# Optimization experiments

Hardware: AMD Instinct MI355X
Metric: run time of the kernel (lower is better)

Reference implementation:

```python
import jax, jax.numpy as jnp
import numpy as np

N_NODES = 50000


def gcn_conv(x, W, b, src, dst, norm, n):
    # x: [N, Fin]; W: [Fin, Fout]; src/dst/norm: [E+N] (self-loops included)
    h = x @ W                                   # dense transform first (PyG order)
    msg = h[src] * norm[:, None]                # gather + per-edge scale
    out = jax.ops.segment_sum(msg, dst, num_segments=n)  # scatter-add aggregate
    return out + b


def setup_inputs() -> dict:
    key = jax.random.key(0)
    k1, k2, k3, k4 = jax.random.split(key, 4)
    F_IN, H, C, E = 64, 64, 16, 800000
    x = jax.random.normal(k1, (N_NODES, F_IN), dtype=jnp.float32)
    edge_index = jax.random.randint(k2, (2, E), 0, N_NODES, dtype=jnp.int64)
    W1 = jax.random.normal(k3, (F_IN, H), dtype=jnp.float32) * (1.0 / np.sqrt(F_IN))
    b1 = jnp.zeros((H,), dtype=jnp.float32)
    W2 = jax.random.normal(k4, (H, C), dtype=jnp.float32) * (1.0 / np.sqrt(H))
    b2 = jnp.zeros((C,), dtype=jnp.float32)
    return {"x": x, "edge_index": edge_index, "W1": W1, "b1": b1, "W2": W2, "b2": b2}


def reference(x, edge_index, W1, b1, W2, b2):
    n = x.shape[0]
    loops = jnp.arange(n, dtype=edge_index.dtype)
    src = jnp.concatenate([edge_index[0], loops])  # GCN adds self-loops
    dst = jnp.concatenate([edge_index[1], loops])
    # symmetric normalization: deg^{-1/2}[src] * deg^{-1/2}[dst], deg over dst
    deg = jax.ops.segment_sum(jnp.ones_like(dst, dtype=x.dtype), dst, num_segments=n)
    dinv = jax.lax.rsqrt(deg)  # deg >= 1 due to self-loops
    norm = dinv[src] * dinv[dst]
    h = gcn_conv(x, W1, b1, src, dst, norm, n)
    h = jax.nn.relu(h)
    out = gcn_conv(h, W2, b2, src, dst, norm, n)
    return out
```

## Files before the change

kernel.cpp:

```cpp
#include <hip/hip_runtime.h>

#define N_NODES 50000
#define N_EDGES 800000
#define F1 64
#define F2 16
#define NBINS 196
#define BIN_SHIFT 8
#define EPB 8192
#define NSB ((N_EDGES + EPB - 1) / EPB)
#define TBW 200
#define STAGE_MAX 6144
#define G1_ROWS 32
#define G1_NB ((N_NODES + G1_ROWS - 1) / G1_ROWS)

typedef _Float16 half_t;
typedef __attribute__((ext_vector_type(8))) _Float16 half8;
typedef __attribute__((ext_vector_type(4))) _Float16 half4;

__global__ void __launch_bounds__(256) k_bs_gemm1(
        const int* __restrict__ src, const int* __restrict__ dst,
        unsigned* __restrict__ pairs, int* __restrict__ table,
        const float* __restrict__ x, const float* __restrict__ W1,
        half_t* __restrict__ h0h) {
    __shared__ int smem[1024 + EPB];
    int t = threadIdx.x;

    if (blockIdx.x < NSB) {
        int* hist    = smem;
        int* loff    = smem + 256;
        int* lcur    = smem + 512;
        int* scanbuf = smem + 768;
        unsigned* stage = (unsigned*)(smem + 1024);
        int blk = blockIdx.x;
        int e0 = blk * EPB;
        int eend = min(e0 + EPB, N_EDGES);
        int n = eend - e0;

        for (int i = t; i < NBINS; i += 256) hist[i] = 0;
        __syncthreads();
        for (int e = e0 + t; e < eend; e += 256)
            atomicAdd(&hist[dst[e] >> BIN_SHIFT], 1);
        __syncthreads();
        int v = (t < NBINS) ? hist[t] : 0;
        scanbuf[t] = v;
        __syncthreads();
        for (int s = 1; s < 256; s <<= 1) {
            int u = (t >= s) ? scanbuf[t - s] : 0;
            __syncthreads();
            scanbuf[t] += u;
            __syncthreads();
        }
        if (t < NBINS) { loff[t] = scanbuf[t] - v; lcur[t] = scanbuf[t] - v; }
        if (t == 0) loff[NBINS] = n;
        __syncthreads();
        for (int e = e0 + t; e < eend; e += 256) {
            int d = dst[e];
            int b = d >> BIN_SHIFT;
            int pos = atomicAdd(&lcur[b], 1);
            stage[pos] = (unsigned)src[e] | ((unsigned)(d & 255) << 16);
        }
        if (t <= NBINS) table[blk * TBW + t] = loff[t];
        __syncthreads();
        for (int i = t; i < n; i += 256) pairs[e0 + i] = stage[i];
    } else {
        float* Ws = (float*)smem;
        int bid = blockIdx.x - NSB;
        int lane = t & 63, wid = t >> 6;
        for (int i = t; i < F1 * F1; i += 256) Ws[i] = W1[i];
        int row0 = bid * G1_ROWS + wid * 8;
        float xv[8], acc[8];
#pragma unroll
        for (int r = 0; r < 8; ++r) {
            int row = row0 + r;
            xv[r] = (row < N_NODES) ? x[row * F1 + lane] : 0.f;
            acc[r] = 0.f;
        }
        __syncthreads();
#pragma unroll
        for (int k = 0; k < F1; ++k) {
            float w = Ws[k * F1 + lane];
#pragma unroll
            for (int r = 0; r < 8; ++r) {
                float xs = __int_as_float(
                    __builtin_amdgcn_readlane(__float_as_int(xv[r]), k));
                acc[r] = fmaf(xs, w, acc[r]);
            }
        }
#pragma unroll
        for (int r = 0; r < 8; ++r) {
            int row = row0 + r;
            if (row < N_NODES) h0h[row * F1 + lane] = (half_t)acc[r];
        }
    }
}

__global__ void __launch_bounds__(256) k_binsort(
        const int* __restrict__ table, const unsigned* __restrict__ pairs,
        float* __restrict__ dinv, int* __restrict__ node_start,
        unsigned short* __restrict__ csr) {
    __shared__ int segoff[NSB];
    __shared__ int segcnt[NSB];
    __shared__ int segdst[NSB];
    __shared__ int scanbuf[256];
    __shared__ int hist[256];
    __shared__ int lcur[256];
    __shared__ unsigned stage[STAGE_MAX];
    __shared__ unsigned short sorted[STAGE_MAX];
    int t = threadIdx.x, b = blockIdx.x;
    int lane = t & 63, wid = t >> 6;

    int c = 0, colsum = 0;
    if (t < NSB) {
        int o = table[t * TBW + b];
        segoff[t] = o;
        colsum = o;
        c = table[t * TBW + b + 1] - o;
        segcnt[t] = c;
    }
    scanbuf[t] = c;
    hist[t] = colsum;
    __syncthreads();
    for (int s = 1; s < 256; s <<= 1) {
        int u  = (t >= s) ? scanbuf[t - s] : 0;
        int u2 = (t >= s) ? hist[t - s] : 0;
        __syncthreads();
        scanbuf[t] += u;
        hist[t] += u2;
        __syncthreads();
    }
    if (t < NSB) segdst[t] = scanbuf[t] - c;
    int n = scanbuf[255];
    int bstart = hist[255];
    __syncthreads();
    hist[t] = 0;
    __syncthreads();

    for (int k = wid; k < NSB; k += 4) {
        int sc = segcnt[k], base = k * EPB + segoff[k], sd = segdst[k];
        for (int i = lane; i < sc; i += 64) stage[sd + i] = pairs[base + i];
    }
    __syncthreads();

    for (int i = t; i < n; i += 256) atomicAdd(&hist[stage[i] >> 16], 1);
    __syncthreads();

    int lo = b << BIN_SHIFT;
    int nb = min(256, N_NODES - lo);
    int hv = hist[t];
    if (t < nb) dinv[lo + t] = rsqrtf(1.0f + (float)hv);
    scanbuf[t] = hv;
    __syncthreads();
    for (int s = 1; s < 256; s <<= 1) {
        int u = (t >= s) ? scanbuf[t - s] : 0;
        __syncthreads();
        scanbuf[t] += u;
        __syncthreads();
    }
    int pr = scanbuf[t] - hv;
    if (t < nb) node_start[lo + t] = bstart + pr;
    if (b == NBINS - 1 && t == 0) node_start[N_NODES] = N_EDGES;
    lcur[t] = pr;
    __syncthreads();

    for (int i = t; i < n; i += 256) {
        unsigned p = stage[i];
        int pos = atomicAdd(&lcur[p >> 16], 1);
        sorted[pos] = (unsigned short)(p & 0xFFFF);
    }
    __syncthreads();
    for (int i = t; i < n; i += 256) csr[bstart + i] = sorted[i];
}

__global__ void __launch_bounds__(256) k_gather1f(
        const int* __restrict__ node_start, const unsigned short* __restrict__ csr,
        const float* __restrict__ dinv, const half8* __restrict__ h08,
        const float* __restrict__ b1, const float* __restrict__ W2,
        half_t* __restrict__ h1h) {
    __shared__ float W2s[F1 * 17];
    __shared__ float b1s[F1];
    __shared__ float rowbuf[4][F1];
    int t = threadIdx.x;
    for (int i = t; i < F1 * F2; i += 256) W2s[(i >> 4) * 17 + (i & 15)] = W2[i];
    if (t < F1) b1s[t] = b1[t];
    __syncthreads();

    int lane = t & 63, wid = t >> 6;
    int j = lane >> 3, f = lane & 7;
    int d = blockIdx.x * 4 + wid;
    int start = node_start[d], end = node_start[d + 1];
    float acc[8] = {0.f, 0.f, 0.f, 0.f, 0.f, 0.f, 0.f, 0.f};
    int i = start + j;
    for (; i + 8 < end; i += 16) {
        int s0 = csr[i], s1 = csr[i + 8];
        float w0 = dinv[s0], w1 = dinv[s1];
        half8 v0 = h08[s0 * 8 + f], v1 = h08[s1 * 8 + f];
#pragma unroll
        for (int q = 0; q < 8; ++q)
            acc[q] += w0 * (float)v0[q] + w1 * (float)v1[q];
    }
    if (i < end) {
        int s = csr[i];
        float w = dinv[s];
        half8 v = h08[s * 8 + f];
#pragma unroll
        for (int q = 0; q < 8; ++q) acc[q] += w * (float)v[q];
    }
#pragma unroll
    for (int m = 8; m <= 32; m <<= 1)
#pragma unroll
        for (int q = 0; q < 8; ++q) acc[q] += __shfl_xor(acc[q], m);

    if (j == 0) {
        float dd = dinv[d];
        half8 sv = h08[d * 8 + f];
#pragma unroll
        for (int q = 0; q < 8; ++q) {
            float r = dd * (acc[q] + dd * (float)sv[q]) + b1s[f * 8 + q];
            rowbuf[wid][f * 8 + q] = fmaxf(r, 0.f);
        }
    }
    __syncthreads();

    int g = lane >> 4, c = lane & 15;
    const float* row = rowbuf[wid];
    float p = 0.f;
#pragma unroll
    for (int kk = 0; kk < 16; ++kk)
        p += row[g * 16 + kk] * W2s[(g * 16 + kk) * 17 + c];
    p += __shfl_xor(p, 16);
    p += __shfl_xor(p, 32);
    if (g == 0) h1h[d * F2 + c] = (half_t)(dinv[d] * p);
}

__global__ void __launch_bounds__(256) k_gather2(
        const int* __restrict__ node_start, const unsigned short* __restrict__ csr,
        const float* __restrict__ dinv, const half4* __restrict__ h14,
        const float4* __restrict__ b24, float4* __restrict__ out4) {
    int t = threadIdx.x;
    int lane = t & 63;
    int j = lane >> 2, f = lane & 3;
    int d = blockIdx.x * 4 + (t >> 6);
    int start = node_start[d], end = node_start[d + 1];
    float acc[4] = {0.f, 0.f, 0.f, 0.f};
    int i = start + j;
    for (; i + 16 < end; i += 32) {
        int s0 = csr[i], s1 = csr[i + 16];
        half4 v0 = h14[s0 * 4 + f], v1 = h14[s1 * 4 + f];
#pragma unroll
        for (int q = 0; q < 4; ++q) acc[q] += (float)v0[q] + (float)v1[q];
    }
    if (i < end) {
        int s = csr[i];
        half4 v = h14[s * 4 + f];
#pragma unroll
        for (int q = 0; q < 4; ++q) acc[q] += (float)v[q];
    }
#pragma unroll
    for (int m = 4; m <= 32; m <<= 1)
#pragma unroll
        for (int q = 0; q < 4; ++q) acc[q] += __shfl_xor(acc[q], m);

    if (j == 0) {
        float dd = dinv[d];
        half4 sv = h14[d * 4 + f];
        float4 bb = b24[f];
        float4 r;
        r.x = bb.x + dd * (acc[0] + (float)sv[0]);
        r.y = bb.y + dd * (acc[1] + (float)sv[1]);
        r.z = bb.z + dd * (acc[2] + (float)sv[2]);
        r.w = bb.w + dd * (acc[3] + (float)sv[3]);
        out4[d * 4 + f] = r;
    }
}

extern "C" void kernel_launch(void* const* d_in, const int* in_sizes, int n_in,
                              void* d_out, int out_size, void* d_ws, size_t ws_size,
                              hipStream_t stream) {
    const float* x  = (const float*)d_in[0];
    const int*   ei = (const int*)d_in[1];
    const float* W1 = (const float*)d_in[2];
    const float* b1 = (const float*)d_in[3];
    const float* W2 = (const float*)d_in[4];
    const float* b2 = (const float*)d_in[5];
    float* out = (float*)d_out;

    const int* src = ei;
    const int* dst = ei + N_EDGES;

    int*            table      = (int*)d_ws;
    float*          dinv       = (float*)d_ws + 40960;
    int*            node_start = (int*)d_ws + 91008;
    unsigned short* csr        = (unsigned short*)((int*)d_ws + 141056);
    unsigned*       pairs      = (unsigned*)d_ws + 541056;
    half_t*         h0h        = (half_t*)((int*)d_ws + 1345056);
    half_t*         h1h        = (half_t*)((int*)d_ws + 2945056);

    k_bs_gemm1<<<NSB + G1_NB, 256, 0, stream>>>(src, dst, pairs, table, x, W1, h0h);
    k_binsort <<<NBINS, 256, 0, stream>>>(table, pairs, dinv, node_start, csr);
    k_gather1f<<<N_NODES / 4, 256, 0, stream>>>(node_start, csr, dinv, (const half8*)h0h,
                                                b1, W2, h1h);
    k_gather2 <<<N_NODES / 4, 256, 0, stream>>>(node_start, csr, dinv, (const half4*)h1h,
                                                (const float4*)b2, (float4*)out);
}
```

Baseline: 169.4 us.

## Fuse bin sort with layer-1 aggregation; compute degrees via global atomics

```diff
diff --git a/kernel.cpp b/kernel.cpp
--- a/kernel.cpp
+++ b/kernel.cpp
@@ -17,11 +17,25 @@
 typedef __attribute__((ext_vector_type(8))) _Float16 half8;
 typedef __attribute__((ext_vector_type(4))) _Float16 half4;
 
+__global__ void __launch_bounds__(256) k_zero(int4* __restrict__ deg4) {
+    int i = blockIdx.x * 256 + threadIdx.x;
+    if (i < (N_NODES + 3) / 4) deg4[i] = int4{0, 0, 0, 0};
+}
+
+__global__ void __launch_bounds__(256) k_cvt(const int* __restrict__ degi,
+                                             float* __restrict__ dinv) {
+    int i = blockIdx.x * 256 + threadIdx.x;
+    if (i < N_NODES) {
+        int v = degi[i];
+        dinv[i] = rsqrtf(1.0f + (float)v);
+    }
+}
+
 __global__ void __launch_bounds__(256) k_bs_gemm1(
         const int* __restrict__ src, const int* __restrict__ dst,
         unsigned* __restrict__ pairs, int* __restrict__ table,
         const float* __restrict__ x, const float* __restrict__ W1,
-        half_t* __restrict__ h0h) {
+        half_t* __restrict__ h0h, int* __restrict__ degi) {
     __shared__ int smem[1024 + EPB];
     int t = threadIdx.x;
 
@@ -38,8 +52,11 @@
 
         for (int i = t; i < NBINS; i += 256) hist[i] = 0;
         __syncthreads();
-        for (int e = e0 + t; e < eend; e += 256)
-            atomicAdd(&hist[dst[e] >> BIN_SHIFT], 1);
+        for (int e = e0 + t; e < eend; e += 256) {
+            int d = dst[e];
+            atomicAdd(&hist[d >> BIN_SHIFT], 1);
+            atomicAdd(&degi[d], 1);
+        }
         __syncthreads();
         int v = (t < NBINS) ? hist[t] : 0;
         scanbuf[t] = v;
@@ -94,142 +111,141 @@
     }
 }
 
-__global__ void __launch_bounds__(256) k_binsort(
+__global__ void __launch_bounds__(1024) k_sort_agg1(
         const int* __restrict__ table, const unsigned* __restrict__ pairs,
-        float* __restrict__ dinv, int* __restrict__ node_start,
-        unsigned short* __restrict__ csr) {
-    __shared__ int segoff[NSB];
-    __shared__ int segcnt[NSB];
-    __shared__ int segdst[NSB];
-    __shared__ int scanbuf[256];
-    __shared__ int hist[256];
-    __shared__ int lcur[256];
+        const float* __restrict__ dinv, int* __restrict__ node_start,
+        unsigned short* __restrict__ csr, const half8* __restrict__ h08,
+        const float* __restrict__ b1, const float* __restrict__ W2,
+        half_t* __restrict__ h1h) {
+    __shared__ int segoff[NSB], segcnt[NSB], segdst[NSB];
+    __shared__ int scanbuf[256], colsum[256], hist[256], lcur[256];
+    __shared__ int nloc[257];
+    __shared__ float dinvs[256];
     __shared__ unsigned stage[STAGE_MAX];
     __shared__ unsigned short sorted[STAGE_MAX];
+    __shared__ float W2s[F1 * 17 + 16];
+    __shared__ float b1s[F1];
+    __shared__ float rowbuf[16][F1];
+
     int t = threadIdx.x, b = blockIdx.x;
     int lane = t & 63, wid = t >> 6;
 
-    int c = 0, colsum = 0;
+    for (int i = t; i < F1 * F2; i += 1024) W2s[(i >> 4) * 17 + (i & 15)] = W2[i];
+    if (t < F1) b1s[t] = b1[t];
+    if (t < 256) hist[t] = 0;
+
+    int c = 0, cs = 0;
     if (t < NSB) {
         int o = table[t * TBW + b];
         segoff[t] = o;
-        colsum = o;
+        cs = o;
         c = table[t * TBW + b + 1] - o;
         segcnt[t] = c;
     }
-    scanbuf[t] = c;
-    hist[t] = colsum;
+    if (t < 256) { scanbuf[t] = c; colsum[t] = cs; }
     __syncthreads();
     for (int s = 1; s < 256; s <<= 1) {
-        int u  = (t >= s) ? scanbuf[t - s] : 0;
-        int u2 = (t >= s) ? hist[t - s] : 0;
-        __syncthreads();
-        scanbuf[t] += u;
-        hist[t] += u2;
+        int u = 0, u2 = 0;
+        if (t < 256 && t >= s) { u = scanbuf[t - s]; u2 = colsum[t - s]; }
+        __syncthreads();
+        if (t < 256) { scanbuf[t] += u; colsum[t] += u2; }
         __syncthreads();
     }
     if (t < NSB) segdst[t] = scanbuf[t] - c;
     int n = scanbuf[255];
-    int bstart = hist[255];
-    __syncthreads();
-    hist[t] = 0;
-    __syncthreads();
-
-    for (int k = wid; k < NSB; k += 4) {
+    int bstart = colsum[255];
+    __syncthreads();
+
+    for (int k = wid; k < NSB; k += 16) {
         int sc = segcnt[k], base = k * EPB + segoff[k], sd = segdst[k];
         for (int i = lane; i < sc; i += 64) stage[sd + i] = pairs[base + i];
     }
     __syncthreads();
 
-    for (int i = t; i < n; i += 256) atomicAdd(&hist[stage[i] >> 16], 1);
+    for (int i = t; i < n; i += 1024) atomicAdd(&hist[stage[i] >> 16], 1);
     __syncthreads();
 
     int lo = b << BIN_SHIFT;
     int nb = min(256, N_NODES - lo);
-    int hv = hist[t];
-    if (t < nb) dinv[lo + t] = rsqrtf(1.0f + (float)hv);
-    scanbuf[t] = hv;
+    int dg = (t < 256) ? hist[t] : 0;
+    if (t < 256) {
+        scanbuf[t] = dg;
+        dinvs[t] = rsqrtf(1.0f + (float)dg);
+    }
     __syncthreads();
     for (int s = 1; s < 256; s <<= 1) {
-        int u = (t >= s) ? scanbuf[t - s] : 0;
-        __syncthreads();
-        scanbuf[t] += u;
-        __syncthreads();
-    }
-    int pr = scanbuf[t] - hv;
-    if (t < nb) node_start[lo + t] = bstart + pr;
+        int u = 0;
+        if (t < 256 && t >= s) u = scanbuf[t - s];
+        __syncthreads();
+        if (t < 256) scanbuf[t] += u;
+        __syncthreads();
+    }
+    if (t < 256) {
+        int pr = scanbuf[t] - dg;
+        nloc[t] = pr;
+        lcur[t] = pr;
+        if (t < nb) node_start[lo + t] = bstart + pr;
+        if (t == 255) nloc[256] = scanbuf[255];
+    }
     if (b == NBINS - 1 && t == 0) node_start[N_NODES] = N_EDGES;
-    lcur[t] = pr;
-    __syncthreads();
-
-    for (int i = t; i < n; i += 256) {
+    __syncthreads();
+
+    for (int i = t; i < n; i += 1024) {
         unsigned p = stage[i];
         int pos = atomicAdd(&lcur[p >> 16], 1);
         sorted[pos] = (unsigned short)(p & 0xFFFF);
     }
     __syncthreads();
-    for (int i = t; i < n; i += 256) csr[bstart + i] = sorted[i];
-}
-
-__global__ void __launch_bounds__(256) k_gather1f(
-        const int* __restrict__ node_start, const unsigned short* __restrict__ csr,
-        const float* __restrict__ dinv, const half8* __restrict__ h08,
-        const float* __restrict__ b1, const float* __restrict__ W2,
-        half_t* __restrict__ h1h) {
-    __shared__ float W2s[F1 * 17];
-    __shared__ float b1s[F1];
-    __shared__ float rowbuf[4][F1];
-    int t = threadIdx.x;
-    for (int i = t; i < F1 * F2; i += 256) W2s[(i >> 4) * 17 + (i & 15)] = W2[i];
-    if (t < F1) b1s[t] = b1[t];
-    __syncthreads();
-
-    int lane = t & 63, wid = t >> 6;
+
+    for (int i = t; i < n; i += 1024) csr[bstart + i] = sorted[i];
+
     int j = lane >> 3, f = lane & 7;
-    int d = blockIdx.x * 4 + wid;
-    int start = node_start[d], end = node_start[d + 1];
-    float acc[8] = {0.f, 0.f, 0.f, 0.f, 0.f, 0.f, 0.f, 0.f};
-    int i = start + j;
-    for (; i + 8 < end; i += 16) {
-        int s0 = csr[i], s1 = csr[i + 8];
-        float w0 = dinv[s0], w1 = dinv[s1];
-        half8 v0 = h08[s0 * 8 + f], v1 = h08[s1 * 8 + f];
-#pragma unroll
-        for (int q = 0; q < 8; ++q)
-            acc[q] += w0 * (float)v0[q] + w1 * (float)v1[q];
-    }
-    if (i < end) {
-        int s = csr[i];
-        float w = dinv[s];
-        half8 v = h08[s * 8 + f];
-#pragma unroll
-        for (int q = 0; q < 8; ++q) acc[q] += w * (float)v[q];
-    }
-#pragma unroll
-    for (int m = 8; m <= 32; m <<= 1)
-#pragma unroll
-        for (int q = 0; q < 8; ++q) acc[q] += __shfl_xor(acc[q], m);
-
-    if (j == 0) {
-        float dd = dinv[d];
-        half8 sv = h08[d * 8 + f];
-#pragma unroll
-        for (int q = 0; q < 8; ++q) {
-            float r = dd * (acc[q] + dd * (float)sv[q]) + b1s[f * 8 + q];
-            rowbuf[wid][f * 8 + q] = fmaxf(r, 0.f);
-        }
-    }
-    __syncthreads();
-
-    int g = lane >> 4, c = lane & 15;
-    const float* row = rowbuf[wid];
-    float p = 0.f;
-#pragma unroll
-    for (int kk = 0; kk < 16; ++kk)
-        p += row[g * 16 + kk] * W2s[(g * 16 + kk) * 17 + c];
-    p += __shfl_xor(p, 16);
-    p += __shfl_xor(p, 32);
-    if (g == 0) h1h[d * F2 + c] = (half_t)(dinv[d] * p);
+    int g = lane >> 4, cc = lane & 15;
+    int qend = min(wid * 16 + 16, nb);
+    for (int q = wid * 16; q < qend; ++q) {
+        int d = lo + q;
+        int i0 = nloc[q], i1 = nloc[q + 1];
+        float acc[8] = {0.f, 0.f, 0.f, 0.f, 0.f, 0.f, 0.f, 0.f};
+        int i = i0 + j;
+        for (; i + 8 < i1; i += 16) {
+            int sA = sorted[i], sB = sorted[i + 8];
+            float wA = dinv[sA], wB = dinv[sB];
+            half8 vA = h08[sA * 8 + f], vB = h08[sB * 8 + f];
+#pragma unroll
+            for (int u = 0; u < 8; ++u)
+                acc[u] += wA * (float)vA[u] + wB * (float)vB[u];
+        }
+        if (i < i1) {
+            int sA = sorted[i];
+            float wA = dinv[sA];
+            half8 vA = h08[sA * 8 + f];
+#pragma unroll
+            for (int u = 0; u < 8; ++u) acc[u] += wA * (float)vA[u];
+        }
+#pragma unroll
+        for (int m = 8; m <= 32; m <<= 1)
+#pragma unroll
+            for (int u = 0; u < 8; ++u) acc[u] += __shfl_xor(acc[u], m);
+
+        float dd = dinvs[q];
+        if (j == 0) {
+            half8 sv = h08[d * 8 + f];
+#pragma unroll
+            for (int u = 0; u < 8; ++u)
+                rowbuf[wid][f * 8 + u] =
+                    fmaxf(dd * (acc[u] + dd * (float)sv[u]) + b1s[f * 8 + u], 0.f);
+        }
+        asm volatile("s_waitcnt lgkmcnt(0)" ::: "memory");
+        __builtin_amdgcn_sched_barrier(0);
+        float p = 0.f;
+#pragma unroll
+        for (int kk = 0; kk < 16; ++kk)
+            p += rowbuf[wid][g * 16 + kk] * W2s[(g * 16 + kk) * 17 + cc];
+        p += __shfl_xor(p, 16);
+        p += __shfl_xor(p, 32);
+        if (g == 0) h1h[d * F2 + cc] = (half_t)(dd * p);
+        asm volatile("" ::: "memory");
+    }
 }
 
 __global__ void __launch_bounds__(256) k_gather2(
@@ -294,11 +310,13 @@
     unsigned*       pairs      = (unsigned*)d_ws + 541056;
     half_t*         h0h        = (half_t*)((int*)d_ws + 1345056);
     half_t*         h1h        = (half_t*)((int*)d_ws + 2945056);
-
-    k_bs_gemm1<<<NSB + G1_NB, 256, 0, stream>>>(src, dst, pairs, table, x, W1, h0h);
-    k_binsort <<<NBINS, 256, 0, stream>>>(table, pairs, dinv, node_start, csr);
-    k_gather1f<<<N_NODES / 4, 256, 0, stream>>>(node_start, csr, dinv, (const half8*)h0h,
-                                                b1, W2, h1h);
+    int*            degi       = (int*)dinv;
+
+    k_zero    <<<49, 256, 0, stream>>>((int4*)degi);
+    k_bs_gemm1<<<NSB + G1_NB, 256, 0, stream>>>(src, dst, pairs, table, x, W1, h0h, degi);
+    k_cvt     <<<196, 256, 0, stream>>>(degi, dinv);
+    k_sort_agg1<<<NBINS, 1024, 0, stream>>>(table, pairs, dinv, node_start, csr,
+                                            (const half8*)h0h, b1, W2, h1h);
     k_gather2 <<<N_NODES / 4, 256, 0, stream>>>(node_start, csr, dinv, (const half4*)h1h,
                                                 (const float4*)b2, (float4*)out);
 }
```

New measurement: 187.1 us. 10.5% more time.
